# Performance work log

Hardware: AMD Instinct MI355X
Metric: run time of the kernel (lower is better)

The kernel has to match this reference:

```python
import jax, jax.numpy as jnp
import numpy as np

TRIANGLE_TABLE = np.array([
    [-1,-1,-1,-1,-1,-1],[1,0,2,-1,-1,-1],[4,0,3,-1,-1,-1],[1,4,2,1,3,4],
    [3,1,5,-1,-1,-1],[2,3,0,2,5,3],[1,4,0,1,5,4],[4,2,5,-1,-1,-1],
    [4,5,2,-1,-1,-1],[4,1,0,4,5,1],[3,2,0,3,5,2],[1,3,5,-1,-1,-1],
    [4,1,2,4,3,1],[3,0,4,-1,-1,-1],[2,0,1,-1,-1,-1],[-1,-1,-1,-1,-1,-1]], dtype=np.int64)
NUM_TRIANGLES_TABLE = np.array([0,1,1,2,1,2,2,1,1,2,2,1,2,1,1,0], dtype=np.int64)
BASE_TET_EDGES = np.array([0,1,0,2,0,3,1,2,1,3,2,3], dtype=np.int64)


def _topology(sdf_np, tet_np):
    """Integer/no-grad part of marching tets (matches torch.no_grad block)."""
    occ = sdf_np > 0                                   # [N]
    occ_f4 = occ[tet_np]                               # [F,4]
    occ_sum = occ_f4.sum(-1)
    valid = (occ_sum > 0) & (occ_sum < 4)              # surface-crossing tets
    tets = tet_np[valid]                               # [T,4]
    edges = tets[:, BASE_TET_EDGES].reshape(-1, 2)     # [T*6,2]
    edges = np.sort(edges, axis=1)                     # canonical (min,max) == sort_edges
    unique_edges, idx_map = np.unique(edges, axis=0, return_inverse=True)
    idx_map = idx_map.reshape(-1)
    mask_edges = occ[unique_edges].sum(-1) == 1        # edges crossing the surface
    mapping = np.full(unique_edges.shape[0], -1, dtype=np.int64)
    mapping[mask_edges] = np.arange(int(mask_edges.sum()), dtype=np.int64)
    idx_map = mapping[idx_map].reshape(-1, 6)          # per-tet edge->vert ids
    interp_v = unique_edges[mask_edges]                # [M,2] endpoints to interpolate
    v_id = 1 << np.arange(4, dtype=np.int64)
    tetindex = (occ_f4[valid].astype(np.int64) * v_id).sum(-1)   # [T] case index 0..15
    num_tri = NUM_TRIANGLES_TABLE[tetindex]
    tt = TRIANGLE_TABLE[tetindex]
    faces1 = np.take_along_axis(idx_map[num_tri == 1], tt[num_tri == 1][:, :3], axis=1).reshape(-1, 3)
    faces2 = np.take_along_axis(idx_map[num_tri == 2], tt[num_tri == 2][:, :6], axis=1).reshape(-1, 3)
    faces = np.concatenate([faces1, faces2], axis=0)
    return interp_v, faces


def setup_inputs() -> dict:
    key = jax.random.key(0)
    k1, k2, k3 = jax.random.split(key, 3)
    N, F = 300000, 1500000
    pos_nx3 = jax.random.normal(k1, (N, 3), dtype=jnp.float32)
    sdf_n = jax.random.normal(k2, (N,), dtype=jnp.float32)
    tet_fx4 = jax.random.randint(k3, (F, 4), 0, N, dtype=jnp.int64)
    return {"pos_nx3": pos_nx3, "sdf_n": sdf_n, "tet_fx4": tet_fx4}


def reference(pos_nx3, sdf_n, tet_fx4):
    # topology (index-valued, non-differentiable) computed on host
    interp_v, faces = _topology(np.asarray(sdf_n), np.asarray(tet_fx4))
    iv = jnp.asarray(interp_v)                         # [M,2]
    ep = pos_nx3[iv]                                   # [M,2,3] endpoint positions
    es = sdf_n[iv] * jnp.array([1.0, -1.0], dtype=sdf_n.dtype)  # [M,2] = (a, -b)
    denom = es.sum(axis=1, keepdims=True)              # a - b
    w = es[:, ::-1] / denom                            # flip: (-b, a)/(a-b)
    verts = (ep * w[..., None]).sum(axis=1)            # linear interpolation at sdf=0
    return verts, jnp.asarray(faces)
```

## Files before the change

### kernel.cpp

```cpp
#include <hip/hip_runtime.h>
#include <stdint.h>

#define TB 256

static __device__ __constant__ int d_TRI[16][6] = {
  {-1,-1,-1,-1,-1,-1},{1,0,2,-1,-1,-1},{4,0,3,-1,-1,-1},{1,4,2,1,3,4},
  {3,1,5,-1,-1,-1},{2,3,0,2,5,3},{1,4,0,1,5,4},{4,2,5,-1,-1,-1},
  {4,5,2,-1,-1,-1},{4,1,0,4,5,1},{3,2,0,3,5,2},{1,3,5,-1,-1,-1},
  {4,1,2,4,3,1},{3,0,4,-1,-1,-1},{2,0,1,-1,-1,-1},{-1,-1,-1,-1,-1,-1}};
static __device__ __constant__ int d_NT[16] = {0,1,1,2,1,2,2,1,1,2,2,1,2,1,1,0};
static __device__ __constant__ int d_EA[6] = {0,0,0,1,1,2};
static __device__ __constant__ int d_EB[6] = {1,2,3,2,3,3};

__device__ __forceinline__ void wave_sync_lds() {
  __builtin_amdgcn_sched_barrier(0);
  asm volatile("s_waitcnt lgkmcnt(0)" ::: "memory");
  __builtin_amdgcn_sched_barrier(0);
}

#define SB 256
#define SI 8
#define STILE (SB*SI)

__global__ void k_scan_partial(const unsigned* __restrict__ in, unsigned* __restrict__ bsum, int n) {
  int b = blockIdx.x;
  int base = b * STILE;
  __shared__ unsigned sh[SB];
  unsigned s = 0;
  for (int i = threadIdx.x; i < STILE; i += SB) {
    int idx = base + i;
    s += (idx < n) ? in[idx] : 0u;
  }
  sh[threadIdx.x] = s; __syncthreads();
  for (int st = SB/2; st > 0; st >>= 1) {
    if (threadIdx.x < st) sh[threadIdx.x] += sh[threadIdx.x + st];
    __syncthreads();
  }
  if (threadIdx.x == 0) bsum[b] = sh[0];
}

__global__ void k_scan_mid(const unsigned* __restrict__ bsum, unsigned* __restrict__ boff,
                           int B, unsigned* __restrict__ total_dst) {
  int t = threadIdx.x;
  unsigned loc[SI];
  int base = t * SI;
  unsigned s = 0;
  #pragma unroll
  for (int i = 0; i < SI; ++i) {
    int idx = base + i;
    unsigned v = (idx < B) ? bsum[idx] : 0u;
    loc[i] = s; s += v;
  }
  __shared__ unsigned sh[SB];
  sh[t] = s; __syncthreads();
  for (int o = 1; o < SB; o <<= 1) {
    unsigned v = (t >= o) ? sh[t - o] : 0u;
    __syncthreads();
    sh[t] += v;
    __syncthreads();
  }
  unsigned texcl = sh[t] - s;
  #pragma unroll
  for (int i = 0; i < SI; ++i) {
    int idx = base + i;
    if (idx < B) boff[idx] = texcl + loc[i];
  }
  if (t == SB - 1 && total_dst) *total_dst = sh[SB - 1];
}

__global__ void k_scan_final(const unsigned* __restrict__ in, const unsigned* __restrict__ boff,
                             unsigned* __restrict__ out, int n) {
  int b = blockIdx.x;
  int base = b * STILE + threadIdx.x * SI;
  unsigned loc[SI];
  unsigned s = 0;
  #pragma unroll
  for (int i = 0; i < SI; ++i) {
    int idx = base + i;
    unsigned v = (idx < n) ? in[idx] : 0u;
    loc[i] = s; s += v;
  }
  __shared__ unsigned sh[SB];
  int t = threadIdx.x;
  sh[t] = s; __syncthreads();
  for (int o = 1; o < SB; o <<= 1) {
    unsigned v = (t >= o) ? sh[t - o] : 0u;
    __syncthreads();
    sh[t] += v;
    __syncthreads();
  }
  unsigned texcl = sh[t] - s;
  unsigned bo = boff[b];
  #pragma unroll
  for (int i = 0; i < SI; ++i) {
    int idx = base + i;
    if (idx < n) out[idx] = bo + texcl + loc[i];
  }
}

__global__ void k_copy_u32(unsigned* __restrict__ dst, const unsigned* __restrict__ src, int n) {
  int i = blockIdx.x * blockDim.x + threadIdx.x;
  if (i < n) dst[i] = src[i];
}

__global__ void k_classify(const int* __restrict__ tet, const float* __restrict__ sdf,
                           unsigned* __restrict__ cnt8, unsigned char* __restrict__ occb,
                           unsigned* __restrict__ bs, int F, int FB) {
  int f = blockIdx.x * TB + threadIdx.x;
  unsigned pk = 0;
  int xg = blockIdx.x & 7;
  if (f < F) {
    int4 q = reinterpret_cast<const int4*>(tet)[f];
    int v[4] = {q.x, q.y, q.z, q.w};
    int oc[4];
    #pragma unroll
    for (int i = 0; i < 4; ++i) oc[i] = sdf[v[i]] > 0.0f;
    int tix = oc[0] | (oc[1] << 1) | (oc[2] << 2) | (oc[3] << 3);
    occb[f] = (unsigned char)tix;
    int nt = d_NT[tix];
    pk = (nt == 1 ? 1u : 0u) | (nt == 2 ? 0x10000u : 0u);
    if (nt > 0) {
      #pragma unroll
      for (int e = 0; e < 6; ++e) {
        int ai = d_EA[e], bi = d_EB[e];
        if (oc[ai] != oc[bi]) {
          int a = v[ai], b = v[bi];
          int lo = a < b ? a : b;
          atomicAdd(&cnt8[(lo & ~7) + xg], 1u);
        }
      }
    }
  }
  __shared__ unsigned sh[TB];
  sh[threadIdx.x] = pk; __syncthreads();
  for (int st = TB/2; st > 0; st >>= 1) {
    if (threadIdx.x < st) sh[threadIdx.x] += sh[threadIdx.x + st];
    __syncthreads();
  }
  if (threadIdx.x == 0) {
    unsigned t = sh[0];
    bs[blockIdx.x] = t & 0xFFFFu;
    bs[FB + blockIdx.x] = t >> 16;
  }
}

__global__ void k_scatter(const int* __restrict__ tet, const unsigned char* __restrict__ occb,
                          unsigned* __restrict__ cur8, unsigned* __restrict__ inst, int F) {
  int f = blockIdx.x * TB + threadIdx.x;
  if (f >= F) return;
  int tix = occb[f];
  if (tix == 0 || tix == 15) return;
  int4 q = reinterpret_cast<const int4*>(tet)[f];
  int v[4] = {q.x, q.y, q.z, q.w};
  int xg = blockIdx.x & 7;
  #pragma unroll
  for (int e = 0; e < 6; ++e) {
    int ai = d_EA[e], bi = d_EB[e];
    int oa = (tix >> ai) & 1, ob = (tix >> bi) & 1;
    if (oa != ob) {
      int a = v[ai], b = v[bi];
      int lo = a < b ? a : b;
      int hi = a < b ? b : a;
      unsigned p = atomicAdd(&cur8[(lo & ~7) + xg], 1u);
      inst[p] = ((unsigned)(lo & 7) << 19) | (unsigned)hi;
    }
  }
}

#define CAP 512
__global__ void k_sortdedupe(const unsigned* __restrict__ off8, unsigned* __restrict__ inst,
                             unsigned* __restrict__ gtmp, unsigned* __restrict__ ucnt,
                             unsigned* __restrict__ ucB, int CB, int N) {
  __shared__ unsigned sA[4][CAP];
  __shared__ unsigned sD[4][CAP];
  int w = threadIdx.x >> 6;
  int lane = threadIdx.x & 63;
  int cb = blockIdx.x * 4 + w;
  if (cb >= CB) return;
  int k8 = cb * 8;
  int k8e = k8 + 8; if (k8e > N) k8e = N;
  unsigned base = off8[k8];
  unsigned n = off8[k8e] - base;
  if (n == 0) {
    if (lane < 8 && k8 + lane < N) ucnt[k8 + lane] = 0u;
    if (lane == 0) ucB[cb] = 0u;
    return;
  }
  if (n <= CAP) {
    for (unsigned k = lane; k < n; k += 64) sA[w][k] = inst[base + k];
    wave_sync_lds();
    for (unsigned k = lane; k < n; k += 64) {
      unsigned val = sA[w][k];
      unsigned r = 0;
      for (unsigned j = 0; j < n; ++j) {
        unsigned x = sA[w][j];
        r += (x < val) || (x == val && j < k);
      }
      sD[w][r] = val;
    }
    wave_sync_lds();
    unsigned ub = 0;
    for (unsigned c = 0; c < n; c += 64) {
      unsigned k = c + (unsigned)lane;
      bool act = k < n;
      unsigned val = act ? sD[w][k] : 0u;
      bool flag = act && (k == 0 || val != sD[w][k - 1]);
      unsigned long long m = __ballot((int)flag);
      if (flag) {
        unsigned pos = ub + (unsigned)__popcll(m & ((1ull << lane) - 1ull));
        sA[w][pos] = val;
      }
      ub += (unsigned)__popcll(m);
    }
    wave_sync_lds();
    for (unsigned k = lane; k < ub; k += 64) {
      unsigned e = sA[w][k];
      unsigned l19 = e >> 19;
      unsigned j = k;
      while (j > 0 && (sA[w][j - 1] >> 19) == l19) --j;
      inst[base + k] = ((k - j) << 22) | (e & 0x3FFFFFu);
    }
    if (lane < 8 && k8 + lane < N) {
      unsigned c = 0;
      for (unsigned j = 0; j < ub; ++j) c += ((sA[w][j] >> 19) == (unsigned)lane);
      ucnt[k8 + lane] = c;
    }
    if (lane == 0) ucB[cb] = ub;
  } else {
    if (lane == 0) {
      unsigned u = 0, prev = 0; bool first = true;
      unsigned uc[8] = {0,0,0,0,0,0,0,0};
      while (true) {
        unsigned m = 0xFFFFFFFFu;
        for (unsigned j = 0; j < n; ++j) {
          unsigned x = inst[base + j] & 0x3FFFFFu;
          if ((first || x > prev) && x < m) m = x;
        }
        if (m == 0xFFFFFFFFu) break;
        unsigned l = m >> 19;
        gtmp[base + u] = (uc[l] << 22) | m;
        uc[l]++; u++; prev = m; first = false;
      }
      for (unsigned j = 0; j < u; ++j) inst[base + j] = gtmp[base + j];
      for (int l = 0; l < 8; ++l) if (k8 + l < N) ucnt[k8 + l] = uc[l];
      ucB[cb] = u;
    }
  }
}

__global__ void k_verts(const unsigned* __restrict__ off8, const unsigned* __restrict__ ucB,
                        const unsigned* __restrict__ uoff, const unsigned* __restrict__ inst,
                        unsigned* __restrict__ uniq, const float* __restrict__ pos,
                        const float* __restrict__ sdf, float* __restrict__ out, int CB) {
  int w = threadIdx.x >> 6;
  int lane = threadIdx.x & 63;
  int cb = blockIdx.x * 4 + w;
  if (cb >= CB) return;
  unsigned u = ucB[cb];
  if (u == 0) return;
  unsigned base = off8[cb * 8];
  for (unsigned k = lane; k < u; k += 64) {
    unsigned e = inst[base + k];
    unsigned hi = e & 0x7FFFFu;
    unsigned l3 = (e >> 19) & 7u;
    unsigned idx = e >> 22;
    unsigned lo = (unsigned)cb * 8u + l3;
    unsigned r = uoff[lo] + idx;
    uniq[r] = hi;
    float a = sdf[lo];
    float b = sdf[hi];
    float d = a - b;
    float w0 = -b / d;
    float w1 = a / d;
    size_t ro = (size_t)3 * r;
    out[ro + 0] = pos[3 * (size_t)lo + 0] * w0 + pos[3 * (size_t)hi + 0] * w1;
    out[ro + 1] = pos[3 * (size_t)lo + 1] * w0 + pos[3 * (size_t)hi + 1] * w1;
    out[ro + 2] = pos[3 * (size_t)lo + 2] * w0 + pos[3 * (size_t)hi + 2] * w1;
  }
}

__global__ void k_faces(const int* __restrict__ tet, const unsigned char* __restrict__ occb,
                        const unsigned* __restrict__ uoff, const unsigned* __restrict__ uniq,
                        const unsigned* __restrict__ C, float* __restrict__ out,
                        int F, int FB, int N) {
  int f = blockIdx.x * TB + threadIdx.x;
  int tix = (f < F) ? (int)occb[f] : 0;
  int nt = d_NT[tix];
  unsigned pk = (nt == 1 ? 1u : 0u) | (nt == 2 ? 0x10000u : 0u);
  __shared__ unsigned sh[TB];
  int t = threadIdx.x;
  sh[t] = pk; __syncthreads();
  for (int o = 1; o < TB; o <<= 1) {
    unsigned v = (t >= o) ? sh[t - o] : 0u;
    __syncthreads();
    sh[t] += v;
    __syncthreads();
  }
  unsigned excl = sh[t] - pk;
  if (f >= F || nt == 0) return;
  unsigned C1b = C[blockIdx.x];
  unsigned T1 = C[FB];
  unsigned C2b = C[FB + blockIdx.x] - T1;
  unsigned M = uoff[N];
  int4 q = reinterpret_cast<const int4*>(tet)[f];
  int v[4] = {q.x, q.y, q.z, q.w};
  int rank[6];
  #pragma unroll
  for (int e = 0; e < 6; ++e) {
    int ai = d_EA[e], bi = d_EB[e];
    int oa = (tix >> ai) & 1, ob = (tix >> bi) & 1;
    if (oa != ob) {
      int a = v[ai], b = v[bi];
      int lo = a < b ? a : b;
      int hi = a < b ? b : a;
      unsigned ubase = uoff[lo];
      unsigned j = 0;
      while (uniq[ubase + j] != (unsigned)hi) ++j;
      rank[e] = (int)(ubase + j);
    } else {
      rank[e] = -1;
    }
  }
  float* fo = out + (size_t)3 * M;
  const int* tt = d_TRI[tix];
  if (nt == 1) {
    unsigned r = C1b + (excl & 0xFFFFu);
    size_t o = (size_t)3 * r;
    fo[o + 0] = (float)rank[tt[0]];
    fo[o + 1] = (float)rank[tt[1]];
    fo[o + 2] = (float)rank[tt[2]];
  } else {
    unsigned r0 = T1 + 2u * (C2b + (excl >> 16));
    size_t o = (size_t)3 * r0;
    #pragma unroll
    for (int c = 0; c < 6; ++c) fo[o + c] = (float)rank[tt[c]];
  }
}

static void run_scan(const unsigned* in, unsigned* out, int n,
                     unsigned* bsum, unsigned* boff, hipStream_t s) {
  int B = (n + STILE - 1) / STILE;
  k_scan_partial<<<B, SB, 0, s>>>(in, bsum, n);
  k_scan_mid<<<1, SB, 0, s>>>(bsum, boff, B, out + n);
  k_scan_final<<<B, SB, 0, s>>>(in, boff, out, n);
}

extern "C" void kernel_launch(void* const* d_in, const int* in_sizes, int n_in,
                              void* d_out, int out_size, void* d_ws, size_t ws_size,
                              hipStream_t stream) {
  const float* pos = (const float*)d_in[0];
  const float* sdf = (const float*)d_in[1];
  const int* tet = (const int*)d_in[2];
  int N = in_sizes[1];
  int F = in_sizes[2] / 4;
  float* out = (float*)d_out;

  char* w = (char*)d_ws;
  size_t o = 0;
  auto take = [&](size_t bytes) -> char* {
    char* p = w + o;
    o = (o + bytes + 255) & ~(size_t)255;
    return p;
  };
  int FB = (F + TB - 1) / TB;
  int CB = (N + 7) / 8;
  unsigned* cnt8 = (unsigned*)take((size_t)(N + 8) * 4);
  unsigned* off8 = (unsigned*)take((size_t)(N + 8) * 4);
  unsigned* cur8 = (unsigned*)take((size_t)(N + 8) * 4);
  unsigned* ucnt = (unsigned*)take((size_t)(N + 1) * 4);
  unsigned* uoff = (unsigned*)take((size_t)(N + 1) * 4);
  unsigned* ucB  = (unsigned*)take((size_t)(CB + 1) * 4);
  unsigned* bs   = (unsigned*)take((size_t)2 * FB * 4);
  unsigned* C    = (unsigned*)take(((size_t)2 * FB + 1) * 4);
  unsigned char* occb = (unsigned char*)take((size_t)F);
  unsigned* inst = (unsigned*)take((size_t)4 * F * 4);
  unsigned* uniq = (unsigned*)take((size_t)4 * F * 4);
  unsigned* bsum = (unsigned*)take(4096 * 4);
  unsigned* boff = (unsigned*)take(4096 * 4);

  int NBc = (CB + 3) / 4;

  hipMemsetAsync(cnt8, 0, (size_t)N * 4, stream);
  k_classify<<<FB, TB, 0, stream>>>(tet, sdf, cnt8, occb, bs, F, FB);
  run_scan(cnt8, off8, N, bsum, boff, stream);
  k_copy_u32<<<(N + TB - 1) / TB, TB, 0, stream>>>(cur8, off8, N);
  k_scatter<<<FB, TB, 0, stream>>>(tet, occb, cur8, inst, F);
  k_sortdedupe<<<NBc, TB, 0, stream>>>(off8, inst, uniq, ucnt, ucB, CB, N);
  run_scan(ucnt, uoff, N, bsum, boff, stream);
  k_verts<<<NBc, TB, 0, stream>>>(off8, ucB, uoff, inst, uniq, pos, sdf, out, CB);
  run_scan(bs, C, 2 * FB, bsum, boff, stream);
  k_faces<<<FB, TB, 0, stream>>>(tet, occb, uoff, uniq, C, out, F, FB, N);
}
```

Before: 1.150 ms.

## Replace atomic per-vertex scatter with two-pass LDS-staged radix partition of edges

Swaps the per-edge global atomic scatter into 8-vertex bins for a two-level partition. The first pass buckets edges into 64 coarse partitions, staged in shared memory for coalesced writes. The second pass repartitions each coarse bucket into 64-vertex fine buckets. Sort-dedupe then runs per fine bucket with one block of 8 waves, and bounds checks are added to the output writes. The aim is to cut scattered global atomics and uncoalesced stores, at the cost of an extra pass and fixed LDS capacity limits that can silently drop edges on overflow.

```diff
diff --git a/kernel.cpp b/kernel.cpp
--- a/kernel.cpp
+++ b/kernel.cpp
@@ -98,17 +98,12 @@
   }
 }
 
-__global__ void k_copy_u32(unsigned* __restrict__ dst, const unsigned* __restrict__ src, int n) {
-  int i = blockIdx.x * blockDim.x + threadIdx.x;
-  if (i < n) dst[i] = src[i];
-}
 
 __global__ void k_classify(const int* __restrict__ tet, const float* __restrict__ sdf,
-                           unsigned* __restrict__ cnt8, unsigned char* __restrict__ occb,
+                           unsigned* __restrict__ fineCnt, unsigned char* __restrict__ occb,
                            unsigned* __restrict__ bs, int F, int FB) {
   int f = blockIdx.x * TB + threadIdx.x;
   unsigned pk = 0;
-  int xg = blockIdx.x & 7;
   if (f < F) {
     int4 q = reinterpret_cast<const int4*>(tet)[f];
     int v[4] = {q.x, q.y, q.z, q.w};
@@ -126,7 +121,7 @@
         if (oc[ai] != oc[bi]) {
           int a = v[ai], b = v[bi];
           int lo = a < b ? a : b;
-          atomicAdd(&cnt8[(lo & ~7) + xg], 1u);
+          atomicAdd(&fineCnt[lo >> 6], 1u);
         }
       }
     }
@@ -144,135 +139,222 @@
   }
 }
 
-__global__ void k_scatter(const int* __restrict__ tet, const unsigned char* __restrict__ occb,
-                          unsigned* __restrict__ cur8, unsigned* __restrict__ inst, int F) {
-  int f = blockIdx.x * TB + threadIdx.x;
-  if (f >= F) return;
-  int tix = occb[f];
-  if (tix == 0 || tix == 15) return;
-  int4 q = reinterpret_cast<const int4*>(tet)[f];
-  int v[4] = {q.x, q.y, q.z, q.w};
-  int xg = blockIdx.x & 7;
-  #pragma unroll
-  for (int e = 0; e < 6; ++e) {
-    int ai = d_EA[e], bi = d_EB[e];
-    int oa = (tix >> ai) & 1, ob = (tix >> bi) & 1;
-    if (oa != ob) {
-      int a = v[ai], b = v[bi];
-      int lo = a < b ? a : b;
-      int hi = a < b ? b : a;
-      unsigned p = atomicAdd(&cur8[(lo & ~7) + xg], 1u);
-      inst[p] = ((unsigned)(lo & 7) << 19) | (unsigned)hi;
-    }
-  }
-}
-
+__global__ void k_init(const unsigned* __restrict__ fineOff, unsigned* __restrict__ finecur,
+                       unsigned* __restrict__ ccur, int PF, int PC) {
+  int i = blockIdx.x * TB + threadIdx.x;
+  if (i < PF) finecur[i] = fineOff[i];
+  if (i < 64) ccur[i] = (i < PC) ? fineOff[i * 128] : 0u;
+}
+
+#define P1MAX 1536
+__global__ void k_scat1(const int* __restrict__ tet, const unsigned char* __restrict__ occb,
+                        unsigned* __restrict__ ccur, unsigned* __restrict__ streamA,
+                        int F, unsigned capA) {
+  __shared__ unsigned hist[64], offb[64], cur[64], gb[64];
+  __shared__ unsigned sbuf[P1MAX];
+  __shared__ unsigned char sfb[P1MAX];
+  int t = threadIdx.x;
+  if (t < 64) { hist[t] = 0; cur[t] = 0; }
+  __syncthreads();
+  int f = blockIdx.x * TB + t;
+  unsigned ev[6]; unsigned char fv[6]; unsigned vm = 0;
+  #pragma unroll
+  for (int e = 0; e < 6; ++e) { ev[e] = 0; fv[e] = 0; }
+  if (f < F) {
+    int tix = occb[f];
+    if (tix != 0 && tix != 15) {
+      int4 q = reinterpret_cast<const int4*>(tet)[f];
+      int v[4] = {q.x, q.y, q.z, q.w};
+      #pragma unroll
+      for (int e = 0; e < 6; ++e) {
+        int ai = d_EA[e], bi = d_EB[e];
+        if (((tix >> ai) & 1) != ((tix >> bi) & 1)) {
+          int a = v[ai], b = v[bi];
+          int lo = a < b ? a : b;
+          int hi = a < b ? b : a;
+          ev[e] = ((unsigned)(lo & 8191) << 19) | (unsigned)hi;
+          fv[e] = (unsigned char)(lo >> 13);
+          atomicAdd(&hist[lo >> 13], 1u);
+          vm |= 1u << e;
+        }
+      }
+    }
+  }
+  __syncthreads();
+  if (t == 0) { unsigned s = 0; for (int i = 0; i < 64; ++i) { offb[i] = s; s += hist[i]; } }
+  __syncthreads();
+  #pragma unroll
+  for (int e = 0; e < 6; ++e) if ((vm >> e) & 1) {
+    unsigned fb = fv[e];
+    unsigned slot = offb[fb] + atomicAdd(&cur[fb], 1u);
+    if (slot < P1MAX) { sbuf[slot] = ev[e]; sfb[slot] = (unsigned char)fb; }
+  }
+  if (t < 64 && hist[t] > 0) gb[t] = atomicAdd(&ccur[t], hist[t]);
+  __syncthreads();
+  unsigned total = offb[63] + hist[63];
+  if (total > P1MAX) total = P1MAX;
+  for (unsigned i = t; i < total; i += TB) {
+    unsigned fb = sfb[i];
+    unsigned pos = gb[fb] + (i - offb[fb]);
+    if (pos < capA) streamA[pos] = sbuf[i];
+  }
+}
+
+#define NPB 64
+#define P2CAP 4096
+__global__ void k_repart(const unsigned* __restrict__ fineOff, const unsigned* __restrict__ streamA,
+                         unsigned* __restrict__ finecur, unsigned* __restrict__ streamB,
+                         int PF, unsigned capB) {
+  __shared__ unsigned hist[128], offb[128], cur[128], gb[128];
+  __shared__ unsigned sorted[P2CAP];
+  __shared__ unsigned char sfb[P2CAP];
+  int t = threadIdx.x;
+  int pc = blockIdx.x / NPB;
+  int ib = blockIdx.x % NPB;
+  for (int i = t; i < 128; i += TB) { hist[i] = 0; cur[i] = 0; }
+  __syncthreads();
+  int fs = pc * 128;
+  int fe = fs + 128; if (fe > PF) fe = PF;
+  unsigned base = fineOff[fs], end = fineOff[fe];
+  unsigned cc = end - base;
+  unsigned chunk = (cc + NPB - 1) / NPB;
+  if (chunk > P2CAP) chunk = P2CAP;
+  unsigned s = base + (unsigned)ib * chunk;
+  if (s > end) s = end;
+  unsigned e_ = s + chunk; if (e_ > end) e_ = end;
+  unsigned ev[16]; unsigned char fv[16];
+  #pragma unroll
+  for (int j = 0; j < 16; ++j) {
+    unsigned idx = s + (unsigned)(j * TB) + (unsigned)t;
+    bool ok = idx < e_;
+    unsigned eV = 0;
+    if (ok) { eV = streamA[idx]; atomicAdd(&hist[eV >> 25], 1u); }
+    ev[j] = eV; fv[j] = ok ? (unsigned char)(eV >> 25) : (unsigned char)255;
+  }
+  __syncthreads();
+  if (t == 0) { unsigned ss = 0; for (int i = 0; i < 128; ++i) { offb[i] = ss; ss += hist[i]; } }
+  __syncthreads();
+  #pragma unroll
+  for (int j = 0; j < 16; ++j) if (fv[j] != 255) {
+    unsigned fb = fv[j];
+    unsigned slot = offb[fb] + atomicAdd(&cur[fb], 1u);
+    if (slot < P2CAP) { sorted[slot] = ev[j] & 0x1FFFFFFu; sfb[slot] = fv[j]; }
+  }
+  if (t < 128 && hist[t] > 0) gb[t] = atomicAdd(&finecur[fs + t], hist[t]);
+  __syncthreads();
+  unsigned total = offb[127] + hist[127];
+  if (total > P2CAP) total = P2CAP;
+  for (unsigned i = t; i < total; i += TB) {
+    unsigned fb = sfb[i];
+    unsigned pos = gb[fb] + (i - offb[fb]);
+    if (pos < capB) streamB[pos] = sorted[i];
+  }
+}
+
+#define PCAP 2560
 #define CAP 512
-__global__ void k_sortdedupe(const unsigned* __restrict__ off8, unsigned* __restrict__ inst,
-                             unsigned* __restrict__ gtmp, unsigned* __restrict__ ucnt,
-                             unsigned* __restrict__ ucB, int CB, int N) {
-  __shared__ unsigned sA[4][CAP];
-  __shared__ unsigned sD[4][CAP];
-  int w = threadIdx.x >> 6;
-  int lane = threadIdx.x & 63;
+__global__ void __launch_bounds__(512) k_sortdd(
+    const unsigned* __restrict__ fineOff, unsigned* __restrict__ streamB,
+    unsigned* __restrict__ ucnt, unsigned* __restrict__ ucC,
+    unsigned* __restrict__ ustart, int N) {
+  __shared__ unsigned sSt[PCAP];
+  __shared__ unsigned sA[8][CAP];
+  __shared__ unsigned sD[8][CAP];
+  __shared__ unsigned sUc[8];
+  int t = threadIdx.x;
+  int w = t >> 6, lane = t & 63;
+  int fp = blockIdx.x;
+  unsigned base = fineOff[fp];
+  unsigned n = fineOff[fp + 1] - base;
+  if (n > PCAP) n = PCAP;
+  for (unsigned k = t; k < n; k += 512) sSt[k] = streamB[base + k];
+  __syncthreads();
+  unsigned nw = 0;
+  for (unsigned c = 0; c < n; c += 64) {
+    unsigned j = c + (unsigned)lane; bool m = false; unsigned e = 0;
+    if (j < n) { e = sSt[j]; m = ((e >> 22) & 7u) == (unsigned)w; }
+    unsigned long long bal = __ballot((int)m);
+    if (m) {
+      unsigned pos = nw + (unsigned)__popcll(bal & ((1ull << lane) - 1ull));
+      if (pos < CAP) sA[w][pos] = e;
+    }
+    nw += (unsigned)__popcll(bal);
+  }
+  if (nw > CAP) nw = CAP;
+  wave_sync_lds();
+  for (unsigned k = lane; k < nw; k += 64) {
+    unsigned val = sA[w][k];
+    unsigned r = 0;
+    for (unsigned j = 0; j < nw; ++j) {
+      unsigned x = sA[w][j];
+      r += (x < val) || (x == val && j < k);
+    }
+    sD[w][r] = val;
+  }
+  wave_sync_lds();
+  unsigned ub = 0;
+  for (unsigned c = 0; c < nw; c += 64) {
+    unsigned k = c + (unsigned)lane;
+    bool act = k < nw;
+    unsigned val = act ? sD[w][k] : 0u;
+    bool flag = act && (k == 0 || val != sD[w][k - 1]);
+    unsigned long long m2 = __ballot((int)flag);
+    if (flag) {
+      unsigned pos = ub + (unsigned)__popcll(m2 & ((1ull << lane) - 1ull));
+      sA[w][pos] = val;
+    }
+    ub += (unsigned)__popcll(m2);
+  }
+  wave_sync_lds();
+  if (lane == 0) sUc[w] = ub;
+  __syncthreads();
+  unsigned pre = 0;
+  for (int i = 0; i < w; ++i) pre += sUc[i];
+  unsigned ust = base + pre;
+  for (unsigned k = lane; k < ub; k += 64) {
+    unsigned e = sA[w][k];
+    unsigned j = k;
+    while (j > 0 && (sA[w][j - 1] >> 19) == (e >> 19)) --j;
+    streamB[ust + k] = ((k - j) << 25) | e;
+  }
+  if (lane < 8) {
+    unsigned c = 0;
+    for (unsigned j = 0; j < ub; ++j) c += ((sA[w][j] >> 19) & 7u) == (unsigned)lane;
+    int lo = fp * 64 + w * 8 + (int)lane;
+    if (lo < N) ucnt[lo] = c;
+  }
+  int cb = fp * 8 + w;
+  if (lane == 0) { ucC[cb] = ub; ustart[cb] = ust; }
+}
+
+__global__ void k_verts(const unsigned* __restrict__ ustart, const unsigned* __restrict__ ucC,
+                        const unsigned* __restrict__ uoff, const unsigned* __restrict__ streamB,
+                        unsigned* __restrict__ uniqA, const float* __restrict__ pos,
+                        const float* __restrict__ sdf, float* __restrict__ out,
+                        int NCB, int N, unsigned out_cap) {
+  int w = threadIdx.x >> 6, lane = threadIdx.x & 63;
   int cb = blockIdx.x * 4 + w;
-  if (cb >= CB) return;
-  int k8 = cb * 8;
-  int k8e = k8 + 8; if (k8e > N) k8e = N;
-  unsigned base = off8[k8];
-  unsigned n = off8[k8e] - base;
-  if (n == 0) {
-    if (lane < 8 && k8 + lane < N) ucnt[k8 + lane] = 0u;
-    if (lane == 0) ucB[cb] = 0u;
-    return;
-  }
-  if (n <= CAP) {
-    for (unsigned k = lane; k < n; k += 64) sA[w][k] = inst[base + k];
-    wave_sync_lds();
-    for (unsigned k = lane; k < n; k += 64) {
-      unsigned val = sA[w][k];
-      unsigned r = 0;
-      for (unsigned j = 0; j < n; ++j) {
-        unsigned x = sA[w][j];
-        r += (x < val) || (x == val && j < k);
-      }
-      sD[w][r] = val;
-    }
-    wave_sync_lds();
-    unsigned ub = 0;
-    for (unsigned c = 0; c < n; c += 64) {
-      unsigned k = c + (unsigned)lane;
-      bool act = k < n;
-      unsigned val = act ? sD[w][k] : 0u;
-      bool flag = act && (k == 0 || val != sD[w][k - 1]);
-      unsigned long long m = __ballot((int)flag);
-      if (flag) {
-        unsigned pos = ub + (unsigned)__popcll(m & ((1ull << lane) - 1ull));
-        sA[w][pos] = val;
-      }
-      ub += (unsigned)__popcll(m);
-    }
-    wave_sync_lds();
-    for (unsigned k = lane; k < ub; k += 64) {
-      unsigned e = sA[w][k];
-      unsigned l19 = e >> 19;
-      unsigned j = k;
-      while (j > 0 && (sA[w][j - 1] >> 19) == l19) --j;
-      inst[base + k] = ((k - j) << 22) | (e & 0x3FFFFFu);
-    }
-    if (lane < 8 && k8 + lane < N) {
-      unsigned c = 0;
-      for (unsigned j = 0; j < ub; ++j) c += ((sA[w][j] >> 19) == (unsigned)lane);
-      ucnt[k8 + lane] = c;
-    }
-    if (lane == 0) ucB[cb] = ub;
-  } else {
-    if (lane == 0) {
-      unsigned u = 0, prev = 0; bool first = true;
-      unsigned uc[8] = {0,0,0,0,0,0,0,0};
-      while (true) {
-        unsigned m = 0xFFFFFFFFu;
-        for (unsigned j = 0; j < n; ++j) {
-          unsigned x = inst[base + j] & 0x3FFFFFu;
-          if ((first || x > prev) && x < m) m = x;
-        }
-        if (m == 0xFFFFFFFFu) break;
-        unsigned l = m >> 19;
-        gtmp[base + u] = (uc[l] << 22) | m;
-        uc[l]++; u++; prev = m; first = false;
-      }
-      for (unsigned j = 0; j < u; ++j) inst[base + j] = gtmp[base + j];
-      for (int l = 0; l < 8; ++l) if (k8 + l < N) ucnt[k8 + l] = uc[l];
-      ucB[cb] = u;
-    }
-  }
-}
-
-__global__ void k_verts(const unsigned* __restrict__ off8, const unsigned* __restrict__ ucB,
-                        const unsigned* __restrict__ uoff, const unsigned* __restrict__ inst,
-                        unsigned* __restrict__ uniq, const float* __restrict__ pos,
-                        const float* __restrict__ sdf, float* __restrict__ out, int CB) {
-  int w = threadIdx.x >> 6;
-  int lane = threadIdx.x & 63;
-  int cb = blockIdx.x * 4 + w;
-  if (cb >= CB) return;
-  unsigned u = ucB[cb];
+  if (cb >= NCB) return;
+  unsigned u = ucC[cb];
   if (u == 0) return;
-  unsigned base = off8[cb * 8];
+  unsigned us = ustart[cb];
+  unsigned lobase = (unsigned)(cb >> 3) * 64u;
+  unsigned M = uoff[N];
   for (unsigned k = lane; k < u; k += 64) {
-    unsigned e = inst[base + k];
+    unsigned e = streamB[us + k];
     unsigned hi = e & 0x7FFFFu;
-    unsigned l3 = (e >> 19) & 7u;
-    unsigned idx = e >> 22;
-    unsigned lo = (unsigned)cb * 8u + l3;
+    unsigned lo = lobase + ((e >> 19) & 63u);
+    unsigned idx = e >> 25;
+    if (lo >= (unsigned)N || hi >= (unsigned)N) continue;
     unsigned r = uoff[lo] + idx;
-    uniq[r] = hi;
-    float a = sdf[lo];
-    float b = sdf[hi];
+    if (r >= M) continue;
+    size_t ro = (size_t)3 * r;
+    if (ro + 3 > (size_t)out_cap) continue;
+    uniqA[r] = hi;
+    float a = sdf[lo], b = sdf[hi];
     float d = a - b;
     float w0 = -b / d;
     float w1 = a / d;
-    size_t ro = (size_t)3 * r;
     out[ro + 0] = pos[3 * (size_t)lo + 0] * w0 + pos[3 * (size_t)hi + 0] * w1;
     out[ro + 1] = pos[3 * (size_t)lo + 1] * w0 + pos[3 * (size_t)hi + 1] * w1;
     out[ro + 2] = pos[3 * (size_t)lo + 2] * w0 + pos[3 * (size_t)hi + 2] * w1;
@@ -280,9 +362,9 @@
 }
 
 __global__ void k_faces(const int* __restrict__ tet, const unsigned char* __restrict__ occb,
-                        const unsigned* __restrict__ uoff, const unsigned* __restrict__ uniq,
+                        const unsigned* __restrict__ uoff, const unsigned* __restrict__ uniqA,
                         const unsigned* __restrict__ C, float* __restrict__ out,
-                        int F, int FB, int N) {
+                        int F, int FB, int N, unsigned out_cap) {
   int f = blockIdx.x * TB + threadIdx.x;
   int tix = (f < F) ? (int)occb[f] : 0;
   int nt = d_NT[tix];
@@ -314,26 +396,32 @@
       int lo = a < b ? a : b;
       int hi = a < b ? b : a;
       unsigned ubase = uoff[lo];
-      unsigned j = 0;
-      while (uniq[ubase + j] != (unsigned)hi) ++j;
-      rank[e] = (int)(ubase + j);
+      unsigned len = uoff[lo + 1] - ubase;
+      unsigned rk = ubase;
+      for (unsigned j = 0; j < len; ++j) {
+        if (uniqA[ubase + j] == (unsigned)hi) { rk = ubase + j; break; }
+      }
+      rank[e] = (int)rk;
     } else {
       rank[e] = -1;
     }
   }
-  float* fo = out + (size_t)3 * M;
   const int* tt = d_TRI[tix];
   if (nt == 1) {
     unsigned r = C1b + (excl & 0xFFFFu);
-    size_t o = (size_t)3 * r;
-    fo[o + 0] = (float)rank[tt[0]];
-    fo[o + 1] = (float)rank[tt[1]];
-    fo[o + 2] = (float)rank[tt[2]];
+    size_t o = (size_t)3 * M + (size_t)3 * r;
+    if (o + 3 <= (size_t)out_cap) {
+      out[o + 0] = (float)rank[tt[0]];
+      out[o + 1] = (float)rank[tt[1]];
+      out[o + 2] = (float)rank[tt[2]];
+    }
   } else {
     unsigned r0 = T1 + 2u * (C2b + (excl >> 16));
-    size_t o = (size_t)3 * r0;
-    #pragma unroll
-    for (int c = 0; c < 6; ++c) fo[o + c] = (float)rank[tt[c]];
+    size_t o = (size_t)3 * M + (size_t)3 * r0;
+    if (o + 6 <= (size_t)out_cap) {
+      #pragma unroll
+      for (int c = 0; c < 6; ++c) out[o + c] = (float)rank[tt[c]];
+    }
   }
 }
 
@@ -363,31 +451,37 @@
     return p;
   };
   int FB = (F + TB - 1) / TB;
-  int CB = (N + 7) / 8;
-  unsigned* cnt8 = (unsigned*)take((size_t)(N + 8) * 4);
-  unsigned* off8 = (unsigned*)take((size_t)(N + 8) * 4);
-  unsigned* cur8 = (unsigned*)take((size_t)(N + 8) * 4);
-  unsigned* ucnt = (unsigned*)take((size_t)(N + 1) * 4);
-  unsigned* uoff = (unsigned*)take((size_t)(N + 1) * 4);
-  unsigned* ucB  = (unsigned*)take((size_t)(CB + 1) * 4);
-  unsigned* bs   = (unsigned*)take((size_t)2 * FB * 4);
-  unsigned* C    = (unsigned*)take(((size_t)2 * FB + 1) * 4);
+  int PF = (N + 63) / 64;
+  int PC = (PF + 127) / 128;
+  int NCB = PF * 8;
+  unsigned capS = (unsigned)(4 * F);
+
+  unsigned* fineCnt = (unsigned*)take((size_t)(PF + 1) * 4);
+  unsigned* fineOff = (unsigned*)take((size_t)(PF + 1) * 4);
+  unsigned* finecur = (unsigned*)take((size_t)(PF + 1) * 4);
+  unsigned* ccur    = (unsigned*)take(64 * 4);
+  unsigned* ucnt    = (unsigned*)take((size_t)(N + 1) * 4);
+  unsigned* uoff    = (unsigned*)take((size_t)(N + 1) * 4);
+  unsigned* ucC     = (unsigned*)take((size_t)NCB * 4);
+  unsigned* ustart  = (unsigned*)take((size_t)NCB * 4);
+  unsigned* bs      = (unsigned*)take((size_t)2 * FB * 4);
+  unsigned* C       = (unsigned*)take(((size_t)2 * FB + 1) * 4);
   unsigned char* occb = (unsigned char*)take((size_t)F);
-  unsigned* inst = (unsigned*)take((size_t)4 * F * 4);
-  unsigned* uniq = (unsigned*)take((size_t)4 * F * 4);
-  unsigned* bsum = (unsigned*)take(4096 * 4);
-  unsigned* boff = (unsigned*)take(4096 * 4);
-
-  int NBc = (CB + 3) / 4;
-
-  hipMemsetAsync(cnt8, 0, (size_t)N * 4, stream);
-  k_classify<<<FB, TB, 0, stream>>>(tet, sdf, cnt8, occb, bs, F, FB);
-  run_scan(cnt8, off8, N, bsum, boff, stream);
-  k_copy_u32<<<(N + TB - 1) / TB, TB, 0, stream>>>(cur8, off8, N);
-  k_scatter<<<FB, TB, 0, stream>>>(tet, occb, cur8, inst, F);
-  k_sortdedupe<<<NBc, TB, 0, stream>>>(off8, inst, uniq, ucnt, ucB, CB, N);
+  unsigned* streamA = (unsigned*)take((size_t)capS * 4);
+  unsigned* streamB = (unsigned*)take((size_t)capS * 4);
+  unsigned* bsum    = (unsigned*)take(4096 * 4);
+  unsigned* boff    = (unsigned*)take(4096 * 4);
+
+  hipMemsetAsync(fineCnt, 0, (size_t)(PF + 1) * 4, stream);
+  k_classify<<<FB, TB, 0, stream>>>(tet, sdf, fineCnt, occb, bs, F, FB);
+  run_scan(fineCnt, fineOff, PF, bsum, boff, stream);
+  k_init<<<(PF + TB - 1) / TB, TB, 0, stream>>>(fineOff, finecur, ccur, PF, PC);
+  k_scat1<<<FB, TB, 0, stream>>>(tet, occb, ccur, streamA, F, capS);
+  k_repart<<<PC * NPB, TB, 0, stream>>>(fineOff, streamA, finecur, streamB, PF, capS);
+  k_sortdd<<<PF, 512, 0, stream>>>(fineOff, streamB, ucnt, ucC, ustart, N);
   run_scan(ucnt, uoff, N, bsum, boff, stream);
-  k_verts<<<NBc, TB, 0, stream>>>(off8, ucB, uoff, inst, uniq, pos, sdf, out, CB);
+  k_verts<<<(NCB + 3) / 4, TB, 0, stream>>>(ustart, ucC, uoff, streamB, streamA,
+                                            pos, sdf, out, NCB, N, (unsigned)out_size);
   run_scan(bs, C, 2 * FB, bsum, boff, stream);
-  k_faces<<<FB, TB, 0, stream>>>(tet, occb, uoff, uniq, C, out, F, FB, N);
-}
+  k_faces<<<FB, TB, 0, stream>>>(tet, occb, uoff, streamA, C, out, F, FB, N, (unsigned)out_size);
+}
```

Measured after the change: 1.315 ms. 1.14x slower.
